# Kernel tuning notes

Hardware: AMD Instinct MI355X
Metric: run time of the kernel (lower is better)

## Reference

```python
import jax, jax.numpy as jnp
import numpy as np

COMMIT_W = 0.25
EMA_DECAY = 0.99
EPS = 1e-5


def setup_inputs() -> dict:
    key = jax.random.key(0)
    k1, k2 = jax.random.split(key)
    B, T, D, K = 16, 1024, 512, 8192
    features = jax.random.normal(k1, (B, T, D), dtype=jnp.float32)
    # __init__ does uniform_(-1/K, 1/K) then ema_weight.copy_(embeddings)
    embeddings = jax.random.uniform(k2, (K, D), dtype=jnp.float32, minval=-1.0 / K, maxval=1.0 / K)
    ema_weight = embeddings
    ema_cluster_size = jnp.ones((K,), dtype=jnp.float32)
    return {"features": features, "embeddings": embeddings,
            "ema_cluster_size": ema_cluster_size, "ema_weight": ema_weight}


def reference(features, embeddings, ema_cluster_size, ema_weight):
    B, T, D = features.shape
    K = embeddings.shape[0]
    flat = features.reshape(-1, D)                      # [N, D]
    # Squared-distance expansion; argmin is identical to argmin of cdist.
    d2 = (jnp.sum(flat * flat, axis=1, keepdims=True)
          - 2.0 * flat @ embeddings.T
          + jnp.sum(embeddings * embeddings, axis=1))   # [N, K]
    indices = jnp.argmin(d2, axis=1)                    # [N]
    quantized = embeddings[indices].reshape(B, T, D)
    # Straight-through estimator
    quantized_st = features + jax.lax.stop_gradient(quantized - features)
    commitment = jnp.mean((features - jax.lax.stop_gradient(quantized_st)) ** 2)
    extra_losses = COMMIT_W * commitment
    # EMA codebook update (training mode); scatter-add instead of one-hot matmul
    ones = jnp.ones(indices.shape, dtype=flat.dtype)
    cluster_size = jax.ops.segment_sum(ones, indices, num_segments=K)          # [K]
    embed_sum = jax.ops.segment_sum(jax.lax.stop_gradient(flat), indices,
                                    num_segments=K)                            # [K, D]
    new_cs = EMA_DECAY * ema_cluster_size + (1.0 - EMA_DECAY) * cluster_size
    new_w = EMA_DECAY * ema_weight + (1.0 - EMA_DECAY) * embed_sum
    cs_norm = (new_cs + EPS) / (jnp.sum(new_cs) + K * EPS)
    new_embeddings = new_w / cs_norm[:, None]
    targets = indices.reshape(B, T)
    return quantized_st, targets, extra_losses, new_embeddings, new_cs, new_w
```

## Files before the change

### kernel.cpp

```cpp
#include <hip/hip_runtime.h>

typedef unsigned short u16;
typedef unsigned int   u32;
typedef unsigned long long u64;

constexpr int NROW  = 16384;
constexpr int DIM   = 512;
constexpr int KCODE = 8192;

constexpr int BM   = 128;
constexpr int BN   = 128;
constexpr int BK   = 32;
constexpr int LSTR = 36;

constexpr size_t Q_OFF = 0;
constexpr size_t T_OFF = 8388608;
constexpr size_t L_OFF = 8404992;
constexpr size_t E_OFF = 8404993;
constexpr size_t C_OFF = 12599297;
constexpr size_t W_OFF = 12607489;

constexpr size_t WS_KEYS   = 0;
constexpr size_t WS_CSIZE  = 131072;
constexpr size_t WS_COMMIT = 163840;
constexpr size_t WS_CSSUM  = 163844;
constexpr size_t WS_XNORM  = 196608;
constexpr size_t WS_ENORM  = 262144;
constexpr size_t WS_ESUM   = 327680;
constexpr size_t WS_NEEDED = WS_ESUM + (size_t)KCODE * DIM * 4;
constexpr size_t WS_FH = WS_NEEDED;
constexpr size_t WS_FL = WS_FH + (size_t)NROW * DIM * 2;
constexpr size_t WS_EH = WS_FL + (size_t)NROW * DIM * 2;
constexpr size_t WS_EL = WS_EH + (size_t)KCODE * DIM * 2;
constexpr size_t WS_BIG = WS_EL + (size_t)KCODE * DIM * 2;

__global__ void rownorm_kernel(const float* __restrict__ src, float* __restrict__ dst) {
    #pragma clang fp contract(off)
    __shared__ float s[4][DIM];
    __shared__ float rr[4][32];
    const int wave = threadIdx.x >> 6, lane = threadIdx.x & 63;
    const int row = blockIdx.x * 4 + wave;
    const float4* p = (const float4*)(src + (size_t)row * DIM);
    float4 v0 = p[lane];
    float4 v1 = p[lane + 64];
    *(float4*)&s[wave][lane * 4] = v0;
    *(float4*)&s[wave][(lane + 64) * 4] = v1;
    __syncthreads();
    if (lane < 32) {
        const int b = lane >> 3, j = lane & 7;
        const float* q = &s[wave][b * 128 + j];
        float x = q[0];
        float r = x * x;
        for (int t = 1; t < 16; ++t) {
            float y = q[8 * t];
            float py = y * y;
            r = r + py;
        }
        rr[wave][lane] = r;
    }
    __syncthreads();
    if (lane == 0) {
        const float* R = rr[wave];
        float B0 = ((R[0] + R[1]) + (R[2] + R[3])) + ((R[4] + R[5]) + (R[6] + R[7]));
        float B1 = ((R[8] + R[9]) + (R[10] + R[11])) + ((R[12] + R[13]) + (R[14] + R[15]));
        float B2 = ((R[16] + R[17]) + (R[18] + R[19])) + ((R[20] + R[21]) + (R[22] + R[23]));
        float B3 = ((R[24] + R[25]) + (R[26] + R[27])) + ((R[28] + R[29]) + (R[30] + R[31]));
        dst[row] = (B0 + B1) + (B2 + B3);
    }
}

typedef short bf16x8 __attribute__((ext_vector_type(8)));
typedef float f32x16 __attribute__((ext_vector_type(16)));

__device__ __forceinline__ bf16x8 frag_of(int4 t) {
    return __builtin_bit_cast(bf16x8, t);
}

__device__ __forceinline__ u32 bf16rne(float x) {
    u32 u = __float_as_uint(x);
    return (u + 0x7fffu + ((u >> 16) & 1u)) >> 16;
}

__device__ __forceinline__ void split4(float4 v, u32& hp0, u32& hp1, u32& lp0, u32& lp1) {
    u32 h0 = bf16rne(v.x), h1 = bf16rne(v.y), h2 = bf16rne(v.z), h3 = bf16rne(v.w);
    hp0 = h0 | (h1 << 16);
    hp1 = h2 | (h3 << 16);
    float r0 = v.x - __uint_as_float(h0 << 16);
    float r1 = v.y - __uint_as_float(h1 << 16);
    float r2 = v.z - __uint_as_float(h2 << 16);
    float r3 = v.w - __uint_as_float(h3 << 16);
    lp0 = bf16rne(r0) | (bf16rne(r1) << 16);
    lp1 = bf16rne(r2) | (bf16rne(r3) << 16);
}

__device__ __forceinline__ u64 packkey(float v, int code) {
    u32 vb = __float_as_uint(v);
    vb = (vb & 0x80000000u) ? ~vb : (vb | 0x80000000u);
    return ((u64)vb << 32) | (u32)code;
}

typedef __attribute__((address_space(1))) const void* gas_ptr;
typedef __attribute__((address_space(3))) void*       las_ptr;
__device__ __forceinline__ void gload16(const void* g, void* l) {
    __builtin_amdgcn_global_load_lds((gas_ptr)(unsigned long long)g,
                                     (las_ptr)(unsigned)(unsigned long long)l,
                                     16, 0, 0);
}

__global__ void split_kernel(const float* __restrict__ src,
                             u16* __restrict__ hi, u16* __restrict__ lo) {
    const size_t i = (size_t)blockIdx.x * 256 + threadIdx.x;
    const float4* p = (const float4*)src;
    float4 a = p[i * 2], b = p[i * 2 + 1];
    u32 ah0, ah1, al0, al1, bh0, bh1, bl0, bl1;
    split4(a, ah0, ah1, al0, al1);
    split4(b, bh0, bh1, bl0, bl1);
    ((uint4*)hi)[i] = make_uint4(ah0, ah1, bh0, bh1);
    ((uint4*)lo)[i] = make_uint4(al0, al1, bl0, bl1);
}

__attribute__((amdgpu_waves_per_eu(2, 2)))
__launch_bounds__(256)
__global__ void argmin_ps_kernel(const u16* __restrict__ fH, const u16* __restrict__ fL,
                                 const u16* __restrict__ eH, const u16* __restrict__ eL,
                                 const float* __restrict__ xnorm,
                                 const float* __restrict__ enorm,
                                 u64* __restrict__ keys) {
    __shared__ int4 sAh[2][512], sAl[2][512], sBh[2][512], sBl[2][512];
    __shared__ float sXn[BM], sEn[BN];

    const int tid = threadIdx.x;
    const int swz = ((int)blockIdx.x & 7) * 1024 + ((int)blockIdx.x >> 3);
    const int cp = swz & 63;
    const int rp = swz >> 6;
    const int row0 = rp * BM;
    const int code0 = cp * BN;

    if (tid < BM) sXn[tid] = xnorm[row0 + tid];
    else          sEn[tid - BM] = enorm[code0 + (tid - BM)];

    const int lane = tid & 63;
    const int wv = tid >> 6;
    const int wr = wv & 1, wc = wv >> 1;
    const int c5 = lane & 31, hgrp = lane >> 5;

    const int4* fH4 = (const int4*)fH;
    const int4* fL4 = (const int4*)fL;
    const int4* eH4 = (const int4*)eH;
    const int4* eL4 = (const int4*)eL;

    size_t goA[2], goB[2];
    int gb[2];
    #pragma unroll
    for (int h = 0; h < 2; ++h) {
        const int g = h * 4 + wv;
        const int i = g * 64 + lane;
        const int r = i >> 8, rb = (i >> 7) & 1, k8 = (i >> 5) & 3, c5i = i & 31;
        const int rl = r * 64 + rb * 32 + c5i;
        goA[h] = (size_t)(row0 + rl) * 64 + k8;
        goB[h] = (size_t)(code0 + rl) * 64 + k8;
        gb[h] = g * 64;
    }

    f32x16 acc[2][2] = {};

    auto STAGE = [&](int buf, int kt) {
        #pragma unroll
        for (int h = 0; h < 2; ++h) {
            gload16(fH4 + goA[h] + kt * 4, (void*)&sAh[buf][gb[h]]);
            gload16(fL4 + goA[h] + kt * 4, (void*)&sAl[buf][gb[h]]);
            gload16(eH4 + goB[h] + kt * 4, (void*)&sBh[buf][gb[h]]);
            gload16(eL4 + goB[h] + kt * 4, (void*)&sBl[buf][gb[h]]);
        }
    };
    auto COMPUTE = [&](int buf) {
        #pragma unroll
        for (int s = 0; s < 2; ++s) {
            const int k8 = s * 2 + hgrp;
            bf16x8 ah[2], al[2], bh[2], bl[2];
            #pragma unroll
            for (int i = 0; i < 2; ++i) {
                ah[i] = frag_of(sAh[buf][((2 * wr + i) * 4 + k8) * 32 + c5]);
                al[i] = frag_of(sAl[buf][((2 * wr + i) * 4 + k8) * 32 + c5]);
                bh[i] = frag_of(sBh[buf][((2 * wc + i) * 4 + k8) * 32 + c5]);
                bl[i] = frag_of(sBl[buf][((2 * wc + i) * 4 + k8) * 32 + c5]);
            }
            #pragma unroll
            for (int i = 0; i < 2; ++i) {
                #pragma unroll
                for (int j = 0; j < 2; ++j) {
                    acc[i][j] = __builtin_amdgcn_mfma_f32_32x32x16_bf16(ah[i], bh[j], acc[i][j], 0, 0, 0);
                    acc[i][j] = __builtin_amdgcn_mfma_f32_32x32x16_bf16(ah[i], bl[j], acc[i][j], 0, 0, 0);
                    acc[i][j] = __builtin_amdgcn_mfma_f32_32x32x16_bf16(al[i], bh[j], acc[i][j], 0, 0, 0);
                }
            }
        }
    };

    STAGE(0, 0);
    STAGE(1, 1);

    int cur = 0;
    #pragma unroll 1
    for (int kt = 0; kt < DIM / BK; ++kt) {
        if (kt < DIM / BK - 1) {
            asm volatile("s_waitcnt vmcnt(8)" ::: "memory");
        } else {
            asm volatile("s_waitcnt vmcnt(0)" ::: "memory");
        }
        __builtin_amdgcn_s_barrier();
        COMPUTE(cur);
        __builtin_amdgcn_s_barrier();
        if (kt + 2 < DIM / BK) STAGE(cur, kt + 2);
        cur ^= 1;
    }

    #pragma unroll
    for (int i = 0; i < 2; ++i) {
        #pragma unroll
        for (int r = 0; r < 16; ++r) {
            const int rowt = 64 * wr + 32 * i + (r & 3) + 8 * (r >> 2) + 4 * hgrp;
            const float xv = sXn[rowt];
            const int ct0 = 64 * wc + c5;
            float v0 = fmaf(-2.0f, acc[i][0][r], xv) + sEn[ct0];
            float v1 = fmaf(-2.0f, acc[i][1][r], xv) + sEn[ct0 + 32];
            u64 ka = packkey(v0, code0 + ct0);
            u64 kb = packkey(v1, code0 + ct0 + 32);
            u64 key = (kb < ka) ? kb : ka;
            #pragma unroll
            for (int m = 1; m < 32; m <<= 1) {
                u64 o = __shfl_xor(key, m, 64);
                if (o < key) key = o;
            }
            if (c5 == 0) atomicMin(&keys[row0 + rowt], key);
        }
    }
}

__launch_bounds__(256, 3)
__global__ void argmin_conv_kernel(const float* __restrict__ feat,
                                   const float* __restrict__ emb,
                                   const float* __restrict__ xnorm,
                                   const float* __restrict__ enorm,
                                   u64* __restrict__ keys) {
    __shared__ u16 sAh[BM][LSTR], sAl[BM][LSTR], sBh[BN][LSTR], sBl[BN][LSTR];
    __shared__ float sXn[BM], sEn[BN];

    const int tid = threadIdx.x;
    const int swz = ((int)blockIdx.x & 7) * 1024 + ((int)blockIdx.x >> 3);
    const int cp = swz & 63;
    const int rp = swz >> 6;
    const int row0 = rp * BM;
    const int code0 = cp * BN;

    if (tid < BM) sXn[tid] = xnorm[row0 + tid];
    else          sEn[tid - BM] = enorm[code0 + (tid - BM)];

    const int srow = tid >> 3;
    const int scol = (tid & 7) * 4;
    const float* aBase = feat + (size_t)row0 * DIM;
    const float* bBase = emb + (size_t)code0 * DIM;

    float4 pa[4], pb[4];
    #pragma unroll
    for (int l = 0; l < 4; ++l) {
        pa[l] = *(const float4*)&aBase[(size_t)(srow + 32 * l) * DIM + scol];
        pb[l] = *(const float4*)&bBase[(size_t)(srow + 32 * l) * DIM + scol];
    }

    const int lane = tid & 63;
    const int wv = tid >> 6;
    const int wr = wv & 1, wc = wv >> 1;
    const int c5 = lane & 31, hgrp = lane >> 5;

    f32x16 acc[2][2] = {};

    #pragma unroll 1
    for (int kt = 0; kt < DIM / BK; ++kt) {
        __syncthreads();
        #pragma unroll
        for (int l = 0; l < 4; ++l) {
            u32 h0, h1, q0, q1;
            split4(pa[l], h0, h1, q0, q1);
            *(uint2*)&sAh[srow + 32 * l][scol] = make_uint2(h0, h1);
            *(uint2*)&sAl[srow + 32 * l][scol] = make_uint2(q0, q1);
            split4(pb[l], h0, h1, q0, q1);
            *(uint2*)&sBh[srow + 32 * l][scol] = make_uint2(h0, h1);
            *(uint2*)&sBl[srow + 32 * l][scol] = make_uint2(q0, q1);
        }
        __syncthreads();
        if (kt + 1 < DIM / BK) {
            const int k0 = (kt + 1) * BK;
            #pragma unroll
            for (int l = 0; l < 4; ++l) {
                pa[l] = *(const float4*)&aBase[(size_t)(srow + 32 * l) * DIM + k0 + scol];
                pb[l] = *(const float4*)&bBase[(size_t)(srow + 32 * l) * DIM + k0 + scol];
            }
        }
        #pragma unroll
        for (int s = 0; s < 2; ++s) {
            const int kk = s * 16 + hgrp * 8;
            bf16x8 ah[2], al[2], bh[2], bl[2];
            #pragma unroll
            for (int i = 0; i < 2; ++i) {
                uint2 a0 = *(const uint2*)&sAh[64 * wr + 32 * i + c5][kk];
                uint2 a1 = *(const uint2*)&sAh[64 * wr + 32 * i + c5][kk + 4];
                ah[i] = frag_of(make_int4(a0.x, a0.y, a1.x, a1.y));
                uint2 c0 = *(const uint2*)&sAl[64 * wr + 32 * i + c5][kk];
                uint2 c1 = *(const uint2*)&sAl[64 * wr + 32 * i + c5][kk + 4];
                al[i] = frag_of(make_int4(c0.x, c0.y, c1.x, c1.y));
                uint2 b0 = *(const uint2*)&sBh[64 * wc + 32 * i + c5][kk];
                uint2 b1 = *(const uint2*)&sBh[64 * wc + 32 * i + c5][kk + 4];
                bh[i] = frag_of(make_int4(b0.x, b0.y, b1.x, b1.y));
                uint2 d0 = *(const uint2*)&sBl[64 * wc + 32 * i + c5][kk];
                uint2 d1 = *(const uint2*)&sBl[64 * wc + 32 * i + c5][kk + 4];
                bl[i] = frag_of(make_int4(d0.x, d0.y, d1.x, d1.y));
            }
            #pragma unroll
            for (int i = 0; i < 2; ++i) {
                #pragma unroll
                for (int j = 0; j < 2; ++j) {
                    acc[i][j] = __builtin_amdgcn_mfma_f32_32x32x16_bf16(ah[i], bh[j], acc[i][j], 0, 0, 0);
                    acc[i][j] = __builtin_amdgcn_mfma_f32_32x32x16_bf16(ah[i], bl[j], acc[i][j], 0, 0, 0);
                    acc[i][j] = __builtin_amdgcn_mfma_f32_32x32x16_bf16(al[i], bh[j], acc[i][j], 0, 0, 0);
                }
            }
        }
    }

    #pragma unroll
    for (int i = 0; i < 2; ++i) {
        #pragma unroll
        for (int r = 0; r < 16; ++r) {
            const int rowt = 64 * wr + 32 * i + (r & 3) + 8 * (r >> 2) + 4 * hgrp;
            const float xv = sXn[rowt];
            const int ct0 = 64 * wc + c5;
            float v0 = fmaf(-2.0f, acc[i][0][r], xv) + sEn[ct0];
            float v1 = fmaf(-2.0f, acc[i][1][r], xv) + sEn[ct0 + 32];
            u64 ka = packkey(v0, code0 + ct0);
            u64 kb = packkey(v1, code0 + ct0 + 32);
            u64 key = (kb < ka) ? kb : ka;
            #pragma unroll
            for (int m = 1; m < 32; m <<= 1) {
                u64 o = __shfl_xor(key, m, 64);
                if (o < key) key = o;
            }
            if (c5 == 0) atomicMin(&keys[row0 + rowt], key);
        }
    }
}

__global__ void gather_kernel(const float* __restrict__ feat,
                              const float* __restrict__ emb,
                              const unsigned long long* __restrict__ keys,
                              float* __restrict__ qout,
                              float* __restrict__ targets,
                              float* __restrict__ esum,
                              float* __restrict__ csize,
                              float* __restrict__ commit) {
    const int row = blockIdx.x;
    const int code = (int)(keys[row] & 0x7fffffffu);
    const int d = threadIdx.x * 2;
    float2 f = *(const float2*)&feat[(size_t)row * DIM + d];
    float2 q = *(const float2*)&emb[(size_t)code * DIM + d];
    float2 qst;
    qst.x = f.x + (q.x - f.x);
    qst.y = f.y + (q.y - f.y);
    *(float2*)&qout[(size_t)row * DIM + d] = qst;
    float dx = f.x - qst.x, dy = f.y - qst.y;
    float local = dx * dx + dy * dy;
    #pragma unroll
    for (int off = 32; off; off >>= 1) local += __shfl_down(local, off, 64);
    __shared__ float wsum[4];
    int lane = threadIdx.x & 63, wv = threadIdx.x >> 6;
    if (lane == 0) wsum[wv] = local;
    __syncthreads();
    if (threadIdx.x == 0) {
        atomicAdd(commit, wsum[0] + wsum[1] + wsum[2] + wsum[3]);
        atomicAdd(&csize[code], 1.0f);
        targets[row] = (float)code;
    }
    atomicAdd(&esum[(size_t)code * DIM + d], f.x);
    atomicAdd(&esum[(size_t)code * DIM + d + 1], f.y);
}

__global__ void newcs_kernel(const float* __restrict__ ema_cs,
                             const float* __restrict__ csize,
                             float* __restrict__ out_cs,
                             float* __restrict__ cs_sum,
                             const float* __restrict__ commit,
                             float* __restrict__ out_loss) {
    int i = blockIdx.x * 256 + threadIdx.x;
    float v = 0.99f * ema_cs[i] + 0.01f * csize[i];
    out_cs[i] = v;
    float s = v;
    #pragma unroll
    for (int off = 32; off; off >>= 1) s += __shfl_down(s, off, 64);
    __shared__ float wsum[4];
    int lane = threadIdx.x & 63, wv = threadIdx.x >> 6;
    if (lane == 0) wsum[wv] = s;
    __syncthreads();
    if (threadIdx.x == 0)
        atomicAdd(cs_sum, wsum[0] + wsum[1] + wsum[2] + wsum[3]);
    if (blockIdx.x == 0 && threadIdx.x == 0)
        out_loss[0] = 0.25f * commit[0] / 8388608.0f;
}

__global__ void final_kernel(const float* __restrict__ ema_w,
                             const float* __restrict__ esum,
                             const float* __restrict__ new_cs,
                             const float* __restrict__ cs_sum,
                             float* __restrict__ out_w,
                             float* __restrict__ out_emb) {
    size_t i4 = ((size_t)blockIdx.x * 256 + threadIdx.x) * 4;
    int k = (int)(i4 >> 9);
    float S = cs_sum[0] + (float)KCODE * 1e-5f;
    float4 es = *(const float4*)&esum[i4];
    float4 ew = *(const float4*)&ema_w[i4];
    float w0 = 0.99f * ew.x + 0.01f * es.x;
    float w1 = 0.99f * ew.y + 0.01f * es.y;
    float w2 = 0.99f * ew.z + 0.01f * es.z;
    float w3 = 0.99f * ew.w + 0.01f * es.w;
    out_w[i4 + 0] = w0; out_w[i4 + 1] = w1; out_w[i4 + 2] = w2; out_w[i4 + 3] = w3;
    float scale = S / (new_cs[k] + 1e-5f);
    out_emb[i4 + 0] = w0 * scale; out_emb[i4 + 1] = w1 * scale;
    out_emb[i4 + 2] = w2 * scale; out_emb[i4 + 3] = w3 * scale;
}

extern "C" void kernel_launch(void* const* d_in, const int* in_sizes, int n_in,
                              void* d_out, int out_size, void* d_ws, size_t ws_size,
                              hipStream_t stream) {
    const float* feat   = (const float*)d_in[0];
    const float* emb    = (const float*)d_in[1];
    const float* ema_cs = (const float*)d_in[2];
    const float* ema_w  = (const float*)d_in[3];
    float* out = (float*)d_out;
    char* ws = (char*)d_ws;
    if (ws_size < WS_NEEDED) return;

    u64* keys     = (u64*)(ws + WS_KEYS);
    float* csize  = (float*)(ws + WS_CSIZE);
    float* commit = (float*)(ws + WS_COMMIT);
    float* cssum  = (float*)(ws + WS_CSSUM);
    float* xnorm  = (float*)(ws + WS_XNORM);
    float* enorm  = (float*)(ws + WS_ENORM);
    float* esum   = (float*)(ws + WS_ESUM);

    (void)hipMemsetAsync(ws + WS_KEYS, 0xFF, (size_t)NROW * 8, stream);
    (void)hipMemsetAsync(ws + WS_CSIZE, 0, WS_CSSUM + 4 - WS_CSIZE, stream);
    (void)hipMemsetAsync(ws + WS_ESUM, 0, (size_t)KCODE * DIM * 4, stream);

    rownorm_kernel<<<NROW / 4, 256, 0, stream>>>(feat, xnorm);
    rownorm_kernel<<<KCODE / 4, 256, 0, stream>>>(emb, enorm);

    if (ws_size >= WS_BIG) {
        u16* fH = (u16*)(ws + WS_FH);
        u16* fL = (u16*)(ws + WS_FL);
        u16* eH = (u16*)(ws + WS_EH);
        u16* eL = (u16*)(ws + WS_EL);
        split_kernel<<<(NROW * DIM) / (256 * 8), 256, 0, stream>>>(feat, fH, fL);
        split_kernel<<<(KCODE * DIM) / (256 * 8), 256, 0, stream>>>(emb, eH, eL);
        argmin_ps_kernel<<<(NROW / BM) * (KCODE / BN), 256, 0, stream>>>(fH, fL, eH, eL,
                                                                         xnorm, enorm, keys);
    } else {
        argmin_conv_kernel<<<(NROW / BM) * (KCODE / BN), 256, 0, stream>>>(feat, emb,
                                                                           xnorm, enorm, keys);
    }

    gather_kernel<<<NROW, 256, 0, stream>>>(feat, emb, keys, out + Q_OFF, out + T_OFF,
                                            esum, csize, commit);
    newcs_kernel<<<KCODE / 256, 256, 0, stream>>>(ema_cs, csize, out + C_OFF, cssum, commit, out + L_OFF);
    final_kernel<<<KCODE * DIM / 1024, 256, 0, stream>>>(ema_w, esum, out + C_OFF, cssum,
                                                         out + W_OFF, out + E_OFF);
}
```

Measured before the change: 1.040 ms.

## Enlarge split-bf16 argmin GEMM tile to 256x256 with 512-thread blocks

Grows the argmin GEMM block tile from 128x128 to 256x256 and uses 8 waves of 512 threads, each wave computing a 128x64 sub-tile with 4x2 MFMA accumulators. The four hi/lo staging buffers are merged into one shared array, and the global-to-LDS load mapping is rebuilt to match. The aim is more data reuse per byte loaded and less global and LDS traffic per MFMA. In exchange it uses more registers (acc grows to 8 tiles) and 128KB of LDS per block, which reduces occupancy, and leaves fewer blocks to balance across CUs.

```diff
diff --git a/kernel.cpp b/kernel.cpp
--- a/kernel.cpp
+++ b/kernel.cpp
@@ -120,28 +120,28 @@
 }
 
 __attribute__((amdgpu_waves_per_eu(2, 2)))
-__launch_bounds__(256)
+__launch_bounds__(512)
 __global__ void argmin_ps_kernel(const u16* __restrict__ fH, const u16* __restrict__ fL,
                                  const u16* __restrict__ eH, const u16* __restrict__ eL,
                                  const float* __restrict__ xnorm,
                                  const float* __restrict__ enorm,
                                  u64* __restrict__ keys) {
-    __shared__ int4 sAh[2][512], sAl[2][512], sBh[2][512], sBl[2][512];
-    __shared__ float sXn[BM], sEn[BN];
+    __shared__ int4 sP[2][4][1024];
+    __shared__ float sXn[256], sEn[256];
 
     const int tid = threadIdx.x;
-    const int swz = ((int)blockIdx.x & 7) * 1024 + ((int)blockIdx.x >> 3);
-    const int cp = swz & 63;
-    const int rp = swz >> 6;
-    const int row0 = rp * BM;
-    const int code0 = cp * BN;
-
-    if (tid < BM) sXn[tid] = xnorm[row0 + tid];
-    else          sEn[tid - BM] = enorm[code0 + (tid - BM)];
+    const int swz = ((int)blockIdx.x & 7) * 256 + ((int)blockIdx.x >> 3);
+    const int cp = swz & 31;
+    const int rp = swz >> 5;
+    const int row0 = rp * 256;
+    const int code0 = cp * 256;
+
+    if (tid < 256) sXn[tid] = xnorm[row0 + tid];
+    else           sEn[tid - 256] = enorm[code0 + (tid - 256)];
 
     const int lane = tid & 63;
     const int wv = tid >> 6;
-    const int wr = wv & 1, wc = wv >> 1;
+    const int wr = wv >> 2, wc = wv & 3;
     const int c5 = lane & 31, hgrp = lane >> 5;
 
     const int4* fH4 = (const int4*)fH;
@@ -149,49 +149,48 @@
     const int4* eH4 = (const int4*)eH;
     const int4* eL4 = (const int4*)eL;
 
-    size_t goA[2], goB[2];
-    int gb[2];
-    #pragma unroll
-    for (int h = 0; h < 2; ++h) {
-        const int g = h * 4 + wv;
-        const int i = g * 64 + lane;
-        const int r = i >> 8, rb = (i >> 7) & 1, k8 = (i >> 5) & 3, c5i = i & 31;
-        const int rl = r * 64 + rb * 32 + c5i;
-        goA[h] = (size_t)(row0 + rl) * 64 + k8;
-        goB[h] = (size_t)(code0 + rl) * 64 + k8;
-        gb[h] = g * 64;
-    }
-
-    f32x16 acc[2][2] = {};
+    const int4* gp[8];
+    int gpl[8], gsb[8];
+    #pragma unroll
+    for (int h = 0; h < 8; ++h) {
+        const int g = wv * 8 + h;
+        const int p = g >> 4;
+        const int gg = g & 15;
+        const int row_local = (gg >> 1) * 32 + c5;
+        const int k8b = (gg & 1) * 2 + hgrp;
+        const int base = (p < 2) ? row0 : code0;
+        const int4* src = (p == 0) ? fH4 : (p == 1) ? fL4 : (p == 2) ? eH4 : eL4;
+        gp[h] = src + (size_t)(base + row_local) * 64 + k8b;
+        gpl[h] = p;
+        gsb[h] = gg * 64 + lane;
+    }
+
+    f32x16 acc[4][2] = {};
 
     auto STAGE = [&](int buf, int kt) {
         #pragma unroll
-        for (int h = 0; h < 2; ++h) {
-            gload16(fH4 + goA[h] + kt * 4, (void*)&sAh[buf][gb[h]]);
-            gload16(fL4 + goA[h] + kt * 4, (void*)&sAl[buf][gb[h]]);
-            gload16(eH4 + goB[h] + kt * 4, (void*)&sBh[buf][gb[h]]);
-            gload16(eL4 + goB[h] + kt * 4, (void*)&sBl[buf][gb[h]]);
-        }
+        for (int h = 0; h < 8; ++h)
+            gload16(gp[h] + kt * 4, (void*)&sP[buf][gpl[h]][gsb[h]]);
     };
     auto COMPUTE = [&](int buf) {
         #pragma unroll
         for (int s = 0; s < 2; ++s) {
             const int k8 = s * 2 + hgrp;
-            bf16x8 ah[2], al[2], bh[2], bl[2];
-            #pragma unroll
-            for (int i = 0; i < 2; ++i) {
-                ah[i] = frag_of(sAh[buf][((2 * wr + i) * 4 + k8) * 32 + c5]);
-                al[i] = frag_of(sAl[buf][((2 * wr + i) * 4 + k8) * 32 + c5]);
-                bh[i] = frag_of(sBh[buf][((2 * wc + i) * 4 + k8) * 32 + c5]);
-                bl[i] = frag_of(sBl[buf][((2 * wc + i) * 4 + k8) * 32 + c5]);
-            }
-            #pragma unroll
-            for (int i = 0; i < 2; ++i) {
+            bf16x8 bh[2], bl[2];
+            #pragma unroll
+            for (int cb = 0; cb < 2; ++cb) {
+                bh[cb] = frag_of(sP[buf][2][(wc * 2 + cb) * 128 + k8 * 32 + c5]);
+                bl[cb] = frag_of(sP[buf][3][(wc * 2 + cb) * 128 + k8 * 32 + c5]);
+            }
+            #pragma unroll
+            for (int rb = 0; rb < 4; ++rb) {
+                bf16x8 ah = frag_of(sP[buf][0][(wr * 4 + rb) * 128 + k8 * 32 + c5]);
+                bf16x8 al = frag_of(sP[buf][1][(wr * 4 + rb) * 128 + k8 * 32 + c5]);
                 #pragma unroll
-                for (int j = 0; j < 2; ++j) {
-                    acc[i][j] = __builtin_amdgcn_mfma_f32_32x32x16_bf16(ah[i], bh[j], acc[i][j], 0, 0, 0);
-                    acc[i][j] = __builtin_amdgcn_mfma_f32_32x32x16_bf16(ah[i], bl[j], acc[i][j], 0, 0, 0);
-                    acc[i][j] = __builtin_amdgcn_mfma_f32_32x32x16_bf16(al[i], bh[j], acc[i][j], 0, 0, 0);
+                for (int cb = 0; cb < 2; ++cb) {
+                    acc[rb][cb] = __builtin_amdgcn_mfma_f32_32x32x16_bf16(ah, bh[cb], acc[rb][cb], 0, 0, 0);
+                    acc[rb][cb] = __builtin_amdgcn_mfma_f32_32x32x16_bf16(ah, bl[cb], acc[rb][cb], 0, 0, 0);
+                    acc[rb][cb] = __builtin_amdgcn_mfma_f32_32x32x16_bf16(al, bh[cb], acc[rb][cb], 0, 0, 0);
                 }
             }
         }
@@ -209,6 +208,7 @@
             asm volatile("s_waitcnt vmcnt(0)" ::: "memory");
         }
         __builtin_amdgcn_s_barrier();
+        asm volatile("" ::: "memory");
         COMPUTE(cur);
         __builtin_amdgcn_s_barrier();
         if (kt + 2 < DIM / BK) STAGE(cur, kt + 2);
@@ -216,14 +216,14 @@
     }
 
     #pragma unroll
-    for (int i = 0; i < 2; ++i) {
+    for (int rb = 0; rb < 4; ++rb) {
         #pragma unroll
         for (int r = 0; r < 16; ++r) {
-            const int rowt = 64 * wr + 32 * i + (r & 3) + 8 * (r >> 2) + 4 * hgrp;
+            const int rowt = wr * 128 + rb * 32 + (r & 3) + 8 * (r >> 2) + 4 * hgrp;
             const float xv = sXn[rowt];
-            const int ct0 = 64 * wc + c5;
-            float v0 = fmaf(-2.0f, acc[i][0][r], xv) + sEn[ct0];
-            float v1 = fmaf(-2.0f, acc[i][1][r], xv) + sEn[ct0 + 32];
+            const int ct0 = wc * 64 + c5;
+            float v0 = fmaf(-2.0f, acc[rb][0][r], xv) + sEn[ct0];
+            float v1 = fmaf(-2.0f, acc[rb][1][r], xv) + sEn[ct0 + 32];
             u64 ka = packkey(v0, code0 + ct0);
             u64 kb = packkey(v1, code0 + ct0 + 32);
             u64 key = (kb < ka) ? kb : ka;
@@ -460,8 +460,8 @@
         u16* eL = (u16*)(ws + WS_EL);
         split_kernel<<<(NROW * DIM) / (256 * 8), 256, 0, stream>>>(feat, fH, fL);
         split_kernel<<<(KCODE * DIM) / (256 * 8), 256, 0, stream>>>(emb, eH, eL);
-        argmin_ps_kernel<<<(NROW / BM) * (KCODE / BN), 256, 0, stream>>>(fH, fL, eH, eL,
-                                                                         xnorm, enorm, keys);
+        argmin_ps_kernel<<<(NROW / 256) * (KCODE / 256), 512, 0, stream>>>(fH, fL, eH, eL,
+                                                                           xnorm, enorm, keys);
     } else {
         argmin_conv_kernel<<<(NROW / BM) * (KCODE / BN), 256, 0, stream>>>(feat, emb,
                                                                            xnorm, enorm, keys);
```

Result: slower. 1.135 ms (+9.2%).
